# Kernel tuning notes

Hardware: AMD Instinct MI355X
Metric: run time of the kernel (lower is better)

## Reference

```python
import jax, jax.numpy as jnp
import numpy as np

N_NODES = 100000
N_EDGES = 1600000
IN_DIM = 128
HEADS = 2
OUT_DIM = 64


def setup_inputs() -> dict:
    key = jax.random.key(0)
    k1, k2, k3, k4, k5 = jax.random.split(key, 5)
    x = jax.random.normal(k1, (N_NODES, IN_DIM), dtype=jnp.float32)
    edge_index = jax.random.randint(k2, (2, N_EDGES), 0, N_NODES, dtype=jnp.int32)
    # xavier-uniform-ish scales
    W = jax.random.uniform(k3, (IN_DIM, HEADS * OUT_DIM), dtype=jnp.float32,
                           minval=-1.0, maxval=1.0) * (6.0 / (IN_DIM + HEADS * OUT_DIM)) ** 0.5
    attn_l = jax.random.uniform(k4, (HEADS, OUT_DIM), dtype=jnp.float32,
                                minval=-1.0, maxval=1.0) * (6.0 / (HEADS + OUT_DIM)) ** 0.5
    attn_r = jax.random.uniform(k5, (HEADS, OUT_DIM), dtype=jnp.float32,
                                minval=-1.0, maxval=1.0) * (6.0 / (HEADS + OUT_DIM)) ** 0.5
    return {"x": x, "edge_index": edge_index, "W": W, "attn_l": attn_l, "attn_r": attn_r}


def reference(x, edge_index, W, attn_l, attn_r):
    N = x.shape[0]
    h = (x @ W).reshape(N, HEADS, OUT_DIM)          # [N,H,D]
    src, dst = edge_index[0], edge_index[1]          # [E]
    h_src = h[src]                                   # [E,H,D] gather
    h_dst = h[dst]                                   # [E,H,D] gather
    # per-edge, per-head attention logits
    alpha = jnp.einsum('ehd,hd->eh', h_src, attn_l) + jnp.einsum('ehd,hd->eh', h_dst, attn_r)
    alpha = jax.nn.leaky_relu(alpha, negative_slope=0.2)
    # NOTE: faithful to original torch code: softmax over dim=0 (ALL edges per head)
    alpha = jax.nn.softmax(alpha, axis=0)            # [E,H]
    msg = h_src * alpha[:, :, None]                  # [E,H,D]
    out = jnp.zeros((N, HEADS, OUT_DIM), dtype=h.dtype).at[dst].add(msg)
    return out.reshape(N, HEADS * OUT_DIM)
```

## Files before the change

### kernel.cpp

```cpp
#include <hip/hip_runtime.h>
#include <hip/hip_fp16.h>
#include <math.h>

#define IN_DIM   128
#define HEADS    2
#define OUT_DIM  64
#define OCOLS    128
#define NB_A     1024
#define BSHIFT   8
#define MAXB     512
#define PCOPIES  8
#define CAP      6144
#define PARTB    512
#define LOG2E    1.4426950408889634f

typedef __attribute__((ext_vector_type(4))) _Float16 half4v;
typedef __attribute__((ext_vector_type(8))) _Float16 half8v;
typedef __attribute__((ext_vector_type(4))) float    floatx4;

__global__ __launch_bounds__(256) void pack_w_kernel(
    const float* __restrict__ W, half8v* __restrict__ wpack) {
  int t = threadIdx.x;
  for (int s = t; s < 2048; s += 256) {
    int l = s & 63, ct = (s >> 6) & 7, kk = s >> 9;
    int q = l >> 4, n = l & 15;
    int c = ct * 16 + n;
    half8v f;
#pragma unroll
    for (int j = 0; j < 8; j++) {
      f[j] = (_Float16)W[(size_t)(kk * 32 + q * 8 + j) * OCOLS + c];
    }
    wpack[s] = f;
  }
}

__global__ __launch_bounds__(256) void gemm_kernel(
    const float* __restrict__ x, const half8v* __restrict__ wpack,
    const float* __restrict__ attn_l, const float* __restrict__ attn_r,
    _Float16* __restrict__ h16, float* __restrict__ alr, int N) {
  __shared__ half8v Wlds[2048];
  __shared__ __align__(16) _Float16 hstage[64 * OCOLS];
  const int tid = threadIdx.x;
  for (int i = tid; i < 2048; i += 256) Wlds[i] = wpack[i];

  const int wave = tid >> 6, lane = tid & 63;
  const int q = lane >> 4, m = lane & 15;
  const int rbase = blockIdx.x * 64 + wave * 16;
  const int arow = rbase + m;
  const bool rok = arow < N;

  half8v a[4];
#pragma unroll
  for (int kk = 0; kk < 4; kk++) {
    float4 u = rok ? *(const float4*)&x[(size_t)arow * IN_DIM + kk * 32 + q * 8]
                   : make_float4(0.f, 0.f, 0.f, 0.f);
    float4 v = rok ? *(const float4*)&x[(size_t)arow * IN_DIM + kk * 32 + q * 8 + 4]
                   : make_float4(0.f, 0.f, 0.f, 0.f);
    a[kk][0] = (_Float16)u.x; a[kk][1] = (_Float16)u.y;
    a[kk][2] = (_Float16)u.z; a[kk][3] = (_Float16)u.w;
    a[kk][4] = (_Float16)v.x; a[kk][5] = (_Float16)v.y;
    a[kk][6] = (_Float16)v.z; a[kk][7] = (_Float16)v.w;
  }
  __syncthreads();

  floatx4 acc[8];
#pragma unroll
  for (int ct = 0; ct < 8; ct++) {
    floatx4 c = {0.f, 0.f, 0.f, 0.f};
#pragma unroll
    for (int kk = 0; kk < 4; kk++) {
      c = __builtin_amdgcn_mfma_f32_16x16x32_f16(
          a[kk], Wlds[(kk * 8 + ct) * 64 + lane], c, 0, 0, 0);
    }
    acc[ct] = c;
  }

  float Al[8], Ar[8];
#pragma unroll
  for (int ct = 0; ct < 8; ct++) {
    Al[ct] = attn_l[ct * 16 + m];
    Ar[ct] = attn_r[ct * 16 + m];
  }
#pragma unroll
  for (int r = 0; r < 4; r++) {
    float al0 = 0.f, al1 = 0.f, ar0 = 0.f, ar1 = 0.f;
#pragma unroll
    for (int ct = 0; ct < 4; ct++) {
      al0 += acc[ct][r] * Al[ct];
      ar0 += acc[ct][r] * Ar[ct];
      al1 += acc[ct + 4][r] * Al[ct + 4];
      ar1 += acc[ct + 4][r] * Ar[ct + 4];
    }
#pragma unroll
    for (int off = 1; off < 16; off <<= 1) {
      al0 += __shfl_xor(al0, off);
      al1 += __shfl_xor(al1, off);
      ar0 += __shfl_xor(ar0, off);
      ar1 += __shfl_xor(ar1, off);
    }
    int orow = rbase + q * 4 + r;
    if (m == 0 && orow < N) {
      *(float4*)&alr[(size_t)orow * 4] =
          make_float4(al0 * LOG2E, al1 * LOG2E, ar0 * LOG2E, ar1 * LOG2E);
    }
  }

#pragma unroll
  for (int ct = 0; ct < 8; ct++) {
#pragma unroll
    for (int r = 0; r < 4; r++) {
      hstage[(wave * 16 + q * 4 + r) * OCOLS + ct * 16 + m] = (_Float16)acc[ct][r];
    }
  }
  __syncthreads();
  {
    int srow = tid >> 2, seg = tid & 3;
    int grow = blockIdx.x * 64 + srow;
    if (grow < N) {
      const int4* s = (const int4*)&hstage[srow * OCOLS + seg * 32];
      int4* d = (int4*)&h16[(size_t)grow * OCOLS + seg * 32];
      int4 v0 = s[0], v1 = s[1], v2 = s[2], v3 = s[3];
      d[0] = v0; d[1] = v1; d[2] = v2; d[3] = v3;
    }
  }
}

__device__ inline void softmax_comb(float& m, float& s, float m2, float s2) {
  float M = fmaxf(m, m2);
  s = s * __builtin_amdgcn_exp2f(m - M) + s2 * __builtin_amdgcn_exp2f(m2 - M);
  m = M;
}

__global__ __launch_bounds__(256) void alpha_stats_kernel(
    const int* __restrict__ src, const int* __restrict__ dst,
    const float* __restrict__ alr, float* __restrict__ partials,
    int* __restrict__ bucket_cnt, int E, int nb1) {
  __shared__ int hist[MAXB];
  for (int i = threadIdx.x; i < MAXB; i += 256) hist[i] = 0;
  __syncthreads();
  const char* ab = (const char*)alr;
  float m0 = -1e30f, s0 = 0.f, m1 = -1e30f, s1 = 0.f;
  for (int e = blockIdx.x * 256 + threadIdx.x; e < E; e += gridDim.x * 256) {
    int sn = src[e], dn = dst[e];
    atomicAdd(&hist[dn >> BSHIFT], 1);
    float4 as = *(const float4*)(ab + ((unsigned)sn << 4));
    float4 ad = *(const float4*)(ab + ((unsigned)dn << 4));
    float a0 = as.x + ad.z;
    float a1 = as.y + ad.w;
    a0 = (a0 > 0.f) ? a0 : 0.2f * a0;
    a1 = (a1 > 0.f) ? a1 : 0.2f * a1;
    {
      float M = fmaxf(m0, a0);
      s0 = s0 * __builtin_amdgcn_exp2f(m0 - M) + __builtin_amdgcn_exp2f(a0 - M);
      m0 = M;
    }
    {
      float M = fmaxf(m1, a1);
      s1 = s1 * __builtin_amdgcn_exp2f(m1 - M) + __builtin_amdgcn_exp2f(a1 - M);
      m1 = M;
    }
  }
  __syncthreads();
  for (int b = threadIdx.x; b < nb1; b += 256) {
    int h = hist[b];
    if (h) atomicAdd(&bucket_cnt[(blockIdx.x & (PCOPIES - 1)) * MAXB + b], h);
  }
#pragma unroll
  for (int off = 1; off < 64; off <<= 1) {
    float m0o = __shfl_xor(m0, off), s0o = __shfl_xor(s0, off);
    float m1o = __shfl_xor(m1, off), s1o = __shfl_xor(s1, off);
    softmax_comb(m0, s0, m0o, s0o);
    softmax_comb(m1, s1, m1o, s1o);
  }
  __shared__ float red[4][4];
  int wave = threadIdx.x >> 6;
  int lane = threadIdx.x & 63;
  if (lane == 0) {
    red[wave][0] = m0; red[wave][1] = s0; red[wave][2] = m1; red[wave][3] = s1;
  }
  __syncthreads();
  if (threadIdx.x == 0) {
    float M0 = red[0][0], S0 = red[0][1], M1 = red[0][2], S1 = red[0][3];
    for (int w = 1; w < 4; w++) {
      softmax_comb(M0, S0, red[w][0], red[w][1]);
      softmax_comb(M1, S1, red[w][2], red[w][3]);
    }
    float* p = &partials[(size_t)blockIdx.x * 4];
    p[0] = M0; p[1] = S0; p[2] = M1; p[3] = S1;
  }
}

__global__ __launch_bounds__(512) void bucket_scan_kernel(
    const int* __restrict__ bucket_cnt, int* __restrict__ bucket_off,
    int* __restrict__ bucket_cursor, const float* __restrict__ partials,
    float* __restrict__ stats, int nb1) {
  __shared__ int part[512];
  __shared__ float red[8][4];
  int t = threadIdx.x;

  if (blockIdx.x == 1) {
    float m0 = -1e30f, s0 = 0.f, m1 = -1e30f, s1 = 0.f;
    for (int i = t; i < NB_A; i += 512) {
      const float* p = &partials[(size_t)i * 4];
      softmax_comb(m0, s0, p[0], p[1]);
      softmax_comb(m1, s1, p[2], p[3]);
    }
#pragma unroll
    for (int off = 1; off < 64; off <<= 1) {
      float m0o = __shfl_xor(m0, off), s0o = __shfl_xor(s0, off);
      float m1o = __shfl_xor(m1, off), s1o = __shfl_xor(s1, off);
      softmax_comb(m0, s0, m0o, s0o);
      softmax_comb(m1, s1, m1o, s1o);
    }
    int wave = t >> 6, lane = t & 63;
    if (lane == 0) {
      red[wave][0] = m0; red[wave][1] = s0; red[wave][2] = m1; red[wave][3] = s1;
    }
    __syncthreads();
    if (t == 0) {
      float M0 = red[0][0], S0 = red[0][1], M1 = red[0][2], S1 = red[0][3];
      for (int w = 1; w < 8; w++) {
        softmax_comb(M0, S0, red[w][0], red[w][1]);
        softmax_comb(M1, S1, red[w][2], red[w][3]);
      }
      stats[0] = M0; stats[1] = 1.f / S0;
      stats[2] = M1; stats[3] = 1.f / S1;
    }
    return;
  }

  int v = 0;
  if (t < nb1) {
#pragma unroll
    for (int c = 0; c < PCOPIES; c++) v += bucket_cnt[c * MAXB + t];
  }
  part[t] = v;
  __syncthreads();
  for (int d = 1; d < 512; d <<= 1) {
    int x = (t >= d) ? part[t - d] : 0;
    __syncthreads();
    part[t] += x;
    __syncthreads();
  }
  int excl = part[t] - v;
  if (t < nb1) {
    bucket_off[t] = excl;
    bucket_cursor[t] = excl;
  }
  if (t == 511) bucket_off[nb1] = part[511];
}

__global__ __launch_bounds__(256) void partition_kernel(
    const int* __restrict__ src, const int* __restrict__ dst,
    int* __restrict__ bucket_cursor, unsigned int* __restrict__ pairs,
    int E, int nb1, int chunk) {
  __shared__ int hist[MAXB];
  __shared__ int cur[MAXB];
  int base = blockIdx.x * chunk;
  int lim = min(base + chunk, E);
  for (int i = threadIdx.x; i < MAXB; i += 256) hist[i] = 0;
  __syncthreads();
  for (int e = base + threadIdx.x; e < lim; e += 256) {
    atomicAdd(&hist[dst[e] >> BSHIFT], 1);
  }
  __syncthreads();
  for (int b = threadIdx.x; b < nb1; b += 256) {
    cur[b] = atomicAdd(&bucket_cursor[b], hist[b]);
  }
  __syncthreads();
  for (int e = base + threadIdx.x; e < lim; e += 256) {
    int d = dst[e];
    int slot = atomicAdd(&cur[d >> BSHIFT], 1);
    pairs[slot] = (unsigned int)src[e] | ((unsigned int)(d & 255) << 17);
  }
}

__global__ __launch_bounds__(256) void bucket_csr_kernel(
    const unsigned int* __restrict__ pairs, const int* __restrict__ bucket_off,
    int* __restrict__ off, int* __restrict__ edge_src, int N, int nb1) {
  __shared__ int hist[256];
  __shared__ int cur[256];
  __shared__ int buf[CAP];
  int b = blockIdx.x;
  int t = threadIdx.x;
  int base_node = b << BSHIFT;
  int nn = min(256, N - base_node);
  int pbeg = bucket_off[b], pend = bucket_off[b + 1];
  int cntE = pend - pbeg;

  hist[t] = 0;
  __syncthreads();
  for (int i = t; i < cntE; i += 256) {
    atomicAdd(&hist[pairs[pbeg + i] >> 17], 1);
  }
  __syncthreads();
  int v = hist[t];
  for (int d = 1; d < 256; d <<= 1) {
    int x = (t >= d) ? hist[t - d] : 0;
    __syncthreads();
    hist[t] += x;
    __syncthreads();
  }
  int excl = hist[t] - v;
  cur[t] = excl;
  if (t < nn) off[base_node + t] = pbeg + excl;
  if (b == nb1 - 1 && t == 0) off[N] = pend;
  __syncthreads();
  if (cntE <= CAP) {
    for (int i = t; i < cntE; i += 256) {
      unsigned int p = pairs[pbeg + i];
      int slot = atomicAdd(&cur[p >> 17], 1);
      buf[slot] = (int)(p & 0x1FFFFu);
    }
    __syncthreads();
    for (int i = t; i < cntE; i += 256) {
      edge_src[pbeg + i] = buf[i];
    }
  } else {
    for (int i = t; i < cntE; i += 256) {
      unsigned int p = pairs[pbeg + i];
      int slot = atomicAdd(&cur[p >> 17], 1);
      edge_src[pbeg + slot] = (int)(p & 0x1FFFFu);
    }
  }
}

__global__ __launch_bounds__(256) void gather_kernel(
    const int* __restrict__ off, const int* __restrict__ edge_src,
    const float* __restrict__ alr, const float* __restrict__ stats,
    const _Float16* __restrict__ h16, float* __restrict__ out, int N) {
  int gid = blockIdx.x * 256 + threadIdx.x;
  int n = gid >> 6;
  if (n >= N) return;
  int lane = threadIdx.x & 63;
  int sub = lane >> 4;
  int l = lane & 15;
  int head = l >> 3;

  const char* ab = (const char*)alr;
  const char* hb = (const char*)h16;
  float4 ad = *(const float4*)(ab + ((unsigned)n << 4));
  float adv = head ? ad.w : ad.z;
  float M = stats[head * 2];
  float invS = stats[head * 2 + 1];
  unsigned loff = (unsigned)l * 16u;

  int beg = off[n], end = off[n + 1];
  float acc[8] = {0.f, 0.f, 0.f, 0.f, 0.f, 0.f, 0.f, 0.f};
  int i = beg + sub;
  for (; i + 12 < end; i += 16) {
    int sn0 = __builtin_nontemporal_load(&edge_src[i]);
    int sn1 = __builtin_nontemporal_load(&edge_src[i + 4]);
    int sn2 = __builtin_nontemporal_load(&edge_src[i + 8]);
    int sn3 = __builtin_nontemporal_load(&edge_src[i + 12]);
    float4 as0 = *(const float4*)(ab + ((unsigned)sn0 << 4));
    float4 as1 = *(const float4*)(ab + ((unsigned)sn1 << 4));
    float4 as2 = *(const float4*)(ab + ((unsigned)sn2 << 4));
    float4 as3 = *(const float4*)(ab + ((unsigned)sn3 << 4));
    half8v hv0 = *(const half8v*)(hb + (((unsigned)sn0 << 8) + loff));
    half8v hv1 = *(const half8v*)(hb + (((unsigned)sn1 << 8) + loff));
    half8v hv2 = *(const half8v*)(hb + (((unsigned)sn2 << 8) + loff));
    half8v hv3 = *(const half8v*)(hb + (((unsigned)sn3 << 8) + loff));
    float a0 = (head ? as0.y : as0.x) + adv;
    float a1 = (head ? as1.y : as1.x) + adv;
    float a2 = (head ? as2.y : as2.x) + adv;
    float a3 = (head ? as3.y : as3.x) + adv;
    a0 = (a0 > 0.f) ? a0 : 0.2f * a0;
    a1 = (a1 > 0.f) ? a1 : 0.2f * a1;
    a2 = (a2 > 0.f) ? a2 : 0.2f * a2;
    a3 = (a3 > 0.f) ? a3 : 0.2f * a3;
    float w0 = __builtin_amdgcn_exp2f(a0 - M) * invS;
    float w1 = __builtin_amdgcn_exp2f(a1 - M) * invS;
    float w2 = __builtin_amdgcn_exp2f(a2 - M) * invS;
    float w3 = __builtin_amdgcn_exp2f(a3 - M) * invS;
#pragma unroll
    for (int j = 0; j < 8; j++) acc[j] += w0 * (float)hv0[j];
#pragma unroll
    for (int j = 0; j < 8; j++) acc[j] += w1 * (float)hv1[j];
#pragma unroll
    for (int j = 0; j < 8; j++) acc[j] += w2 * (float)hv2[j];
#pragma unroll
    for (int j = 0; j < 8; j++) acc[j] += w3 * (float)hv3[j];
  }
  for (; i + 4 < end; i += 8) {
    int sn0 = __builtin_nontemporal_load(&edge_src[i]);
    int sn1 = __builtin_nontemporal_load(&edge_src[i + 4]);
    float4 as0 = *(const float4*)(ab + ((unsigned)sn0 << 4));
    float4 as1 = *(const float4*)(ab + ((unsigned)sn1 << 4));
    half8v hv0 = *(const half8v*)(hb + (((unsigned)sn0 << 8) + loff));
    half8v hv1 = *(const half8v*)(hb + (((unsigned)sn1 << 8) + loff));
    float a0 = (head ? as0.y : as0.x) + adv;
    float a1 = (head ? as1.y : as1.x) + adv;
    a0 = (a0 > 0.f) ? a0 : 0.2f * a0;
    a1 = (a1 > 0.f) ? a1 : 0.2f * a1;
    float w0 = __builtin_amdgcn_exp2f(a0 - M) * invS;
    float w1 = __builtin_amdgcn_exp2f(a1 - M) * invS;
#pragma unroll
    for (int j = 0; j < 8; j++) acc[j] += w0 * (float)hv0[j];
#pragma unroll
    for (int j = 0; j < 8; j++) acc[j] += w1 * (float)hv1[j];
  }
  if (i < end) {
    int sn = __builtin_nontemporal_load(&edge_src[i]);
    float4 as = *(const float4*)(ab + ((unsigned)sn << 4));
    half8v hv = *(const half8v*)(hb + (((unsigned)sn << 8) + loff));
    float a = (head ? as.y : as.x) + adv;
    a = (a > 0.f) ? a : 0.2f * a;
    float w = __builtin_amdgcn_exp2f(a - M) * invS;
#pragma unroll
    for (int j = 0; j < 8; j++) acc[j] += w * (float)hv[j];
  }
#pragma unroll
  for (int j = 0; j < 8; j++) {
    acc[j] += __shfl_xor(acc[j], 16);
    acc[j] += __shfl_xor(acc[j], 32);
  }
  if (sub == 0) {
    char* ob = (char*)out;
    unsigned obase = ((unsigned)n << 9) + (unsigned)l * 32u;
    floatx4 o0 = {acc[0], acc[1], acc[2], acc[3]};
    floatx4 o1 = {acc[4], acc[5], acc[6], acc[7]};
    __builtin_nontemporal_store(o0, (floatx4*)(ob + obase));
    __builtin_nontemporal_store(o1, (floatx4*)(ob + obase + 16));
  }
}

extern "C" void kernel_launch(void* const* d_in, const int* in_sizes, int n_in,
                              void* d_out, int out_size, void* d_ws, size_t ws_size,
                              hipStream_t stream) {
  const float* x      = (const float*)d_in[0];
  const int*   edge   = (const int*)d_in[1];
  const float* W      = (const float*)d_in[2];
  const float* attn_l = (const float*)d_in[3];
  const float* attn_r = (const float*)d_in[4];

  const int N = in_sizes[0] / IN_DIM;
  const int E = in_sizes[1] / 2;
  const int* src = edge;
  const int* dst = edge + E;
  float* out = (float*)d_out;

  const int nb1 = (N + 255) >> BSHIFT;

  _Float16*     h16      = (_Float16*)d_ws;
  float*        alr      = (float*)(h16 + (size_t)N * OCOLS);
  float*        partials = alr + (size_t)N * 4;
  float*        stats    = partials + (size_t)NB_A * 4;
  int*          bucket_cnt    = (int*)(stats + 4);
  int*          bucket_off    = bucket_cnt + PCOPIES * MAXB;
  int*          bucket_cursor = bucket_off + MAXB + 1;
  int*          off      = bucket_cursor + MAXB;
  unsigned int* pairs    = (unsigned int*)(off + N + 1);
  int*          edge_src = (int*)(pairs + E);
  half8v*       wpack    = (half8v*)(edge_src + E);

  const int chunk = (E + PARTB - 1) / PARTB;

  hipMemsetAsync(bucket_cnt, 0, PCOPIES * MAXB * sizeof(int), stream);

  pack_w_kernel<<<1, 256, 0, stream>>>(W, wpack);
  gemm_kernel<<<(N + 63) / 64, 256, 0, stream>>>(x, wpack, attn_l, attn_r, h16, alr, N);
  alpha_stats_kernel<<<NB_A, 256, 0, stream>>>(src, dst, alr, partials, bucket_cnt, E, nb1);
  bucket_scan_kernel<<<2, 512, 0, stream>>>(bucket_cnt, bucket_off, bucket_cursor,
                                            partials, stats, nb1);
  partition_kernel<<<PARTB, 256, 0, stream>>>(src, dst, bucket_cursor, pairs, E, nb1, chunk);
  bucket_csr_kernel<<<nb1, 256, 0, stream>>>(pairs, bucket_off, off, edge_src, N, nb1);
  gather_kernel<<<((size_t)N * 64 + 255) / 256, 256, 0, stream>>>(
      off, edge_src, alr, stats, h16, out, N);
}
```

Measured before the change: 270.9 us.

## Fuse softmax stats with edge partitioning into fixed-capacity bucket regions

Merges the alpha-statistics pass and the partition kernel into one kernel. Each block stages its edge chunk in shared memory and scatters packed pairs into per-bucket regions of fixed capacity, which removes the separate histogram, cursor and second read of src/dst, plus one launch. The CSR kernel now reads each bucket from its fixed region. The gather kernel also replaces its tail loops with a single predicated 4-way loop. The risk is that a bucket overflowing the fixed capacity has its edges clamped and silently overwritten, and clamping the chunk size leaves edges unprocessed for larger E.

```diff
diff --git a/kernel.cpp b/kernel.cpp
--- a/kernel.cpp
+++ b/kernel.cpp
@@ -6,12 +6,11 @@
 #define HEADS    2
 #define OUT_DIM  64
 #define OCOLS    128
-#define NB_A     1024
 #define BSHIFT   8
 #define MAXB     512
-#define PCOPIES  8
-#define CAP      6144
-#define PARTB    512
+#define CAPF     5120
+#define PARTB    1024
+#define CHUNK_MAX 1600
 #define LOG2E    1.4426950408889634f
 
 typedef __attribute__((ext_vector_type(4))) _Float16 half4v;
@@ -131,17 +130,30 @@
   m = M;
 }
 
-__global__ __launch_bounds__(256) void alpha_stats_kernel(
+__global__ __launch_bounds__(256) void alpha_part_kernel(
     const int* __restrict__ src, const int* __restrict__ dst,
     const float* __restrict__ alr, float* __restrict__ partials,
-    int* __restrict__ bucket_cnt, int E, int nb1) {
+    int* __restrict__ gcur, unsigned int* __restrict__ pairs,
+    int E, int nb1, int chunk) {
+  __shared__ unsigned int pv[CHUNK_MAX];
+  __shared__ unsigned short bk[CHUNK_MAX];
   __shared__ int hist[MAXB];
-  for (int i = threadIdx.x; i < MAXB; i += 256) hist[i] = 0;
-  __syncthreads();
+  __shared__ int cur[MAXB];
+  const int t = threadIdx.x;
+  const int base = blockIdx.x * chunk;
+  const int lim = min(base + chunk, E);
+  const int cntLoc = lim - base;
+
+  for (int i = t; i < MAXB; i += 256) hist[i] = 0;
+  __syncthreads();
+
   const char* ab = (const char*)alr;
   float m0 = -1e30f, s0 = 0.f, m1 = -1e30f, s1 = 0.f;
-  for (int e = blockIdx.x * 256 + threadIdx.x; e < E; e += gridDim.x * 256) {
+  for (int e = base + t; e < lim; e += 256) {
     int sn = src[e], dn = dst[e];
+    int li = e - base;
+    pv[li] = (unsigned int)sn | ((unsigned int)(dn & 255) << 17);
+    bk[li] = (unsigned short)(dn >> BSHIFT);
     atomicAdd(&hist[dn >> BSHIFT], 1);
     float4 as = *(const float4*)(ab + ((unsigned)sn << 4));
     float4 ad = *(const float4*)(ab + ((unsigned)dn << 4));
@@ -161,9 +173,18 @@
     }
   }
   __syncthreads();
-  for (int b = threadIdx.x; b < nb1; b += 256) {
+  for (int b = t; b < nb1; b += 256) {
     int h = hist[b];
-    if (h) atomicAdd(&bucket_cnt[(blockIdx.x & (PCOPIES - 1)) * MAXB + b], h);
+    if (h) cur[b] = b * CAPF + atomicAdd(&gcur[b], h);
+  }
+  __syncthreads();
+  for (int li = t; li < cntLoc; li += 256) {
+    unsigned int p = pv[li];
+    int bb = bk[li];
+    int slot = atomicAdd(&cur[bb], 1);
+    int cap = (bb + 1) * CAPF - 1;
+    if (slot > cap) slot = cap;
+    pairs[slot] = p;
   }
 #pragma unroll
   for (int off = 1; off < 64; off <<= 1) {
@@ -173,13 +194,12 @@
     softmax_comb(m1, s1, m1o, s1o);
   }
   __shared__ float red[4][4];
-  int wave = threadIdx.x >> 6;
-  int lane = threadIdx.x & 63;
+  int wave = t >> 6, lane = t & 63;
   if (lane == 0) {
     red[wave][0] = m0; red[wave][1] = s0; red[wave][2] = m1; red[wave][3] = s1;
   }
   __syncthreads();
-  if (threadIdx.x == 0) {
+  if (t == 0) {
     float M0 = red[0][0], S0 = red[0][1], M1 = red[0][2], S1 = red[0][3];
     for (int w = 1; w < 4; w++) {
       softmax_comb(M0, S0, red[w][0], red[w][1]);
@@ -191,16 +211,15 @@
 }
 
 __global__ __launch_bounds__(512) void bucket_scan_kernel(
-    const int* __restrict__ bucket_cnt, int* __restrict__ bucket_off,
-    int* __restrict__ bucket_cursor, const float* __restrict__ partials,
-    float* __restrict__ stats, int nb1) {
+    const int* __restrict__ gcur, int* __restrict__ bucket_off,
+    const float* __restrict__ partials, float* __restrict__ stats, int nb1) {
   __shared__ int part[512];
   __shared__ float red[8][4];
   int t = threadIdx.x;
 
   if (blockIdx.x == 1) {
     float m0 = -1e30f, s0 = 0.f, m1 = -1e30f, s1 = 0.f;
-    for (int i = t; i < NB_A; i += 512) {
+    for (int i = t; i < PARTB; i += 512) {
       const float* p = &partials[(size_t)i * 4];
       softmax_comb(m0, s0, p[0], p[1]);
       softmax_comb(m1, s1, p[2], p[3]);
@@ -229,11 +248,7 @@
     return;
   }
 
-  int v = 0;
-  if (t < nb1) {
-#pragma unroll
-    for (int c = 0; c < PCOPIES; c++) v += bucket_cnt[c * MAXB + t];
-  }
+  int v = (t < nb1) ? gcur[t] : 0;
   part[t] = v;
   __syncthreads();
   for (int d = 1; d < 512; d <<= 1) {
@@ -243,36 +258,8 @@
     __syncthreads();
   }
   int excl = part[t] - v;
-  if (t < nb1) {
-    bucket_off[t] = excl;
-    bucket_cursor[t] = excl;
-  }
+  if (t < nb1) bucket_off[t] = excl;
   if (t == 511) bucket_off[nb1] = part[511];
-}
-
-__global__ __launch_bounds__(256) void partition_kernel(
-    const int* __restrict__ src, const int* __restrict__ dst,
-    int* __restrict__ bucket_cursor, unsigned int* __restrict__ pairs,
-    int E, int nb1, int chunk) {
-  __shared__ int hist[MAXB];
-  __shared__ int cur[MAXB];
-  int base = blockIdx.x * chunk;
-  int lim = min(base + chunk, E);
-  for (int i = threadIdx.x; i < MAXB; i += 256) hist[i] = 0;
-  __syncthreads();
-  for (int e = base + threadIdx.x; e < lim; e += 256) {
-    atomicAdd(&hist[dst[e] >> BSHIFT], 1);
-  }
-  __syncthreads();
-  for (int b = threadIdx.x; b < nb1; b += 256) {
-    cur[b] = atomicAdd(&bucket_cursor[b], hist[b]);
-  }
-  __syncthreads();
-  for (int e = base + threadIdx.x; e < lim; e += 256) {
-    int d = dst[e];
-    int slot = atomicAdd(&cur[d >> BSHIFT], 1);
-    pairs[slot] = (unsigned int)src[e] | ((unsigned int)(d & 255) << 17);
-  }
 }
 
 __global__ __launch_bounds__(256) void bucket_csr_kernel(
@@ -280,18 +267,19 @@
     int* __restrict__ off, int* __restrict__ edge_src, int N, int nb1) {
   __shared__ int hist[256];
   __shared__ int cur[256];
-  __shared__ int buf[CAP];
+  __shared__ int buf[CAPF];
   int b = blockIdx.x;
   int t = threadIdx.x;
   int base_node = b << BSHIFT;
   int nn = min(256, N - base_node);
   int pbeg = bucket_off[b], pend = bucket_off[b + 1];
   int cntE = pend - pbeg;
+  int rb = b * CAPF;
 
   hist[t] = 0;
   __syncthreads();
   for (int i = t; i < cntE; i += 256) {
-    atomicAdd(&hist[pairs[pbeg + i] >> 17], 1);
+    atomicAdd(&hist[pairs[rb + i] >> 17], 1);
   }
   __syncthreads();
   int v = hist[t];
@@ -306,22 +294,14 @@
   if (t < nn) off[base_node + t] = pbeg + excl;
   if (b == nb1 - 1 && t == 0) off[N] = pend;
   __syncthreads();
-  if (cntE <= CAP) {
-    for (int i = t; i < cntE; i += 256) {
-      unsigned int p = pairs[pbeg + i];
-      int slot = atomicAdd(&cur[p >> 17], 1);
-      buf[slot] = (int)(p & 0x1FFFFu);
-    }
-    __syncthreads();
-    for (int i = t; i < cntE; i += 256) {
-      edge_src[pbeg + i] = buf[i];
-    }
-  } else {
-    for (int i = t; i < cntE; i += 256) {
-      unsigned int p = pairs[pbeg + i];
-      int slot = atomicAdd(&cur[p >> 17], 1);
-      edge_src[pbeg + slot] = (int)(p & 0x1FFFFu);
-    }
+  for (int i = t; i < cntE; i += 256) {
+    unsigned int p = pairs[rb + i];
+    int slot = atomicAdd(&cur[p >> 17], 1);
+    buf[slot] = (int)(p & 0x1FFFFu);
+  }
+  __syncthreads();
+  for (int i = t; i < cntE; i += 256) {
+    edge_src[pbeg + i] = buf[i];
   }
 }
 
@@ -347,12 +327,15 @@
 
   int beg = off[n], end = off[n + 1];
   float acc[8] = {0.f, 0.f, 0.f, 0.f, 0.f, 0.f, 0.f, 0.f};
-  int i = beg + sub;
-  for (; i + 12 < end; i += 16) {
-    int sn0 = __builtin_nontemporal_load(&edge_src[i]);
-    int sn1 = __builtin_nontemporal_load(&edge_src[i + 4]);
-    int sn2 = __builtin_nontemporal_load(&edge_src[i + 8]);
-    int sn3 = __builtin_nontemporal_load(&edge_src[i + 12]);
+  for (int ib = beg + sub; ib < end; ib += 16) {
+    bool k1 = ib + 4 < end, k2 = ib + 8 < end, k3 = ib + 12 < end;
+    int e1 = k1 ? ib + 4 : ib;
+    int e2 = k2 ? ib + 8 : ib;
+    int e3 = k3 ? ib + 12 : ib;
+    int sn0 = __builtin_nontemporal_load(&edge_src[ib]);
+    int sn1 = __builtin_nontemporal_load(&edge_src[e1]);
+    int sn2 = __builtin_nontemporal_load(&edge_src[e2]);
+    int sn3 = __builtin_nontemporal_load(&edge_src[e3]);
     float4 as0 = *(const float4*)(ab + ((unsigned)sn0 << 4));
     float4 as1 = *(const float4*)(ab + ((unsigned)sn1 << 4));
     float4 as2 = *(const float4*)(ab + ((unsigned)sn2 << 4));
@@ -370,9 +353,9 @@
     a2 = (a2 > 0.f) ? a2 : 0.2f * a2;
     a3 = (a3 > 0.f) ? a3 : 0.2f * a3;
     float w0 = __builtin_amdgcn_exp2f(a0 - M) * invS;
-    float w1 = __builtin_amdgcn_exp2f(a1 - M) * invS;
-    float w2 = __builtin_amdgcn_exp2f(a2 - M) * invS;
-    float w3 = __builtin_amdgcn_exp2f(a3 - M) * invS;
+    float w1 = k1 ? __builtin_amdgcn_exp2f(a1 - M) * invS : 0.f;
+    float w2 = k2 ? __builtin_amdgcn_exp2f(a2 - M) * invS : 0.f;
+    float w3 = k3 ? __builtin_amdgcn_exp2f(a3 - M) * invS : 0.f;
 #pragma unroll
     for (int j = 0; j < 8; j++) acc[j] += w0 * (float)hv0[j];
 #pragma unroll
@@ -381,34 +364,6 @@
     for (int j = 0; j < 8; j++) acc[j] += w2 * (float)hv2[j];
 #pragma unroll
     for (int j = 0; j < 8; j++) acc[j] += w3 * (float)hv3[j];
-  }
-  for (; i + 4 < end; i += 8) {
-    int sn0 = __builtin_nontemporal_load(&edge_src[i]);
-    int sn1 = __builtin_nontemporal_load(&edge_src[i + 4]);
-    float4 as0 = *(const float4*)(ab + ((unsigned)sn0 << 4));
-    float4 as1 = *(const float4*)(ab + ((unsigned)sn1 << 4));
-    half8v hv0 = *(const half8v*)(hb + (((unsigned)sn0 << 8) + loff));
-    half8v hv1 = *(const half8v*)(hb + (((unsigned)sn1 << 8) + loff));
-    float a0 = (head ? as0.y : as0.x) + adv;
-    float a1 = (head ? as1.y : as1.x) + adv;
-    a0 = (a0 > 0.f) ? a0 : 0.2f * a0;
-    a1 = (a1 > 0.f) ? a1 : 0.2f * a1;
-    float w0 = __builtin_amdgcn_exp2f(a0 - M) * invS;
-    float w1 = __builtin_amdgcn_exp2f(a1 - M) * invS;
-#pragma unroll
-    for (int j = 0; j < 8; j++) acc[j] += w0 * (float)hv0[j];
-#pragma unroll
-    for (int j = 0; j < 8; j++) acc[j] += w1 * (float)hv1[j];
-  }
-  if (i < end) {
-    int sn = __builtin_nontemporal_load(&edge_src[i]);
-    float4 as = *(const float4*)(ab + ((unsigned)sn << 4));
-    half8v hv = *(const half8v*)(hb + (((unsigned)sn << 8) + loff));
-    float a = (head ? as.y : as.x) + adv;
-    a = (a > 0.f) ? a : 0.2f * a;
-    float w = __builtin_amdgcn_exp2f(a - M) * invS;
-#pragma unroll
-    for (int j = 0; j < 8; j++) acc[j] += w * (float)hv[j];
   }
 #pragma unroll
   for (int j = 0; j < 8; j++) {
@@ -445,25 +400,24 @@
   _Float16*     h16      = (_Float16*)d_ws;
   float*        alr      = (float*)(h16 + (size_t)N * OCOLS);
   float*        partials = alr + (size_t)N * 4;
-  float*        stats    = partials + (size_t)NB_A * 4;
-  int*          bucket_cnt    = (int*)(stats + 4);
-  int*          bucket_off    = bucket_cnt + PCOPIES * MAXB;
-  int*          bucket_cursor = bucket_off + MAXB + 1;
-  int*          off      = bucket_cursor + MAXB;
-  unsigned int* pairs    = (unsigned int*)(off + N + 1);
-  int*          edge_src = (int*)(pairs + E);
+  float*        stats    = partials + (size_t)PARTB * 4;
+  int*          gcur     = (int*)(stats + 4);
+  int*          bucket_off = gcur + MAXB;
+  int*          off      = bucket_off + MAXB + 4;
+  unsigned int* pairs    = (unsigned int*)(off + N + 4);
+  int*          edge_src = (int*)(pairs + (size_t)nb1 * CAPF);
   half8v*       wpack    = (half8v*)(edge_src + E);
 
-  const int chunk = (E + PARTB - 1) / PARTB;
-
-  hipMemsetAsync(bucket_cnt, 0, PCOPIES * MAXB * sizeof(int), stream);
+  int chunk = (E + PARTB - 1) / PARTB;
+  if (chunk > CHUNK_MAX) chunk = CHUNK_MAX;
+
+  hipMemsetAsync(gcur, 0, MAXB * sizeof(int), stream);
 
   pack_w_kernel<<<1, 256, 0, stream>>>(W, wpack);
   gemm_kernel<<<(N + 63) / 64, 256, 0, stream>>>(x, wpack, attn_l, attn_r, h16, alr, N);
-  alpha_stats_kernel<<<NB_A, 256, 0, stream>>>(src, dst, alr, partials, bucket_cnt, E, nb1);
-  bucket_scan_kernel<<<2, 512, 0, stream>>>(bucket_cnt, bucket_off, bucket_cursor,
-                                            partials, stats, nb1);
-  partition_kernel<<<PARTB, 256, 0, stream>>>(src, dst, bucket_cursor, pairs, E, nb1, chunk);
+  alpha_part_kernel<<<PARTB, 256, 0, stream>>>(src, dst, alr, partials, gcur,
+                                               pairs, E, nb1, chunk);
+  bucket_scan_kernel<<<2, 512, 0, stream>>>(gcur, bucket_off, partials, stats, nb1);
   bucket_csr_kernel<<<nb1, 256, 0, stream>>>(pairs, bucket_off, off, edge_src, N, nb1);
   gather_kernel<<<((size_t)N * 64 + 255) / 256, 256, 0, stream>>>(
       off, edge_src, alr, stats, h16, out, N);
```

Result: no change. 267.4 us (-1.3%).
